# Kernel tuning notes

Hardware: AMD Instinct MI355X
Metric: run time of the kernel (lower is better)

The kernel has to match this reference:

```python
import jax, jax.numpy as jnp
import numpy as np

NUM_HEADS = 4

def setup_inputs() -> dict:
    key = jax.random.key(0)
    ks = jax.random.split(key, 5)
    B, T, F, C = 2, 128, 256, 256
    # weights scaled ~1/sqrt(C) so softmax is not saturated
    s = 1.0 / np.sqrt(C)
    return {
        "x": jax.random.normal(ks[0], (B, T, F, C), jnp.float32),
        "w_in": jax.random.normal(ks[1], (3 * C, C), jnp.float32) * s,
        "b_in": jax.random.normal(ks[2], (3 * C,), jnp.float32) * 0.01,
        "w_out": jax.random.normal(ks[3], (C, C), jnp.float32) * s,
        "b_out": jax.random.normal(ks[4], (C,), jnp.float32) * 0.01,
        "band": 16,
    }

def reference(x, w_in, b_in, w_out, b_out, band):
    B, T, F, C = x.shape
    H = NUM_HEADS
    D = C // H
    x2 = x.reshape(B * T, F, C)  # attention over frequency, independent per (B,T)
    qkv = x2 @ w_in.T + b_in  # [BT, F, 3C]
    q, k, v = jnp.split(qkv, 3, axis=-1)
    def heads(t):
        return t.reshape(B * T, F, H, D).transpose(0, 2, 1, 3)  # [BT, H, F, D]
    q, k, v = heads(q), heads(k), heads(v)
    scores = jnp.einsum('bhid,bhjd->bhij', q, k) / jnp.sqrt(jnp.asarray(D, x.dtype))
    i = jnp.arange(F)[:, None]
    j = jnp.arange(F)[None, :]
    keep = jnp.abs(i - j) <= band  # banded locality mask [F, F]
    scores = jnp.where(keep, scores, -jnp.inf)
    attn = jax.nn.softmax(scores, axis=-1)
    out = jnp.einsum('bhij,bhjd->bhid', attn, v)  # [BT, H, F, D]
    out = out.transpose(0, 2, 1, 3).reshape(B * T, F, C)
    y = out @ w_out.T + b_out
    return y.reshape(B, T, F, C)
```

## Files before the change

kernel.cpp:

```cpp
#include <hip/hip_runtime.h>
#include <hip/hip_bf16.h>
#include <cstdint>

typedef unsigned int u32;
typedef __attribute__((ext_vector_type(8))) __bf16 bf16x8;
typedef __attribute__((ext_vector_type(4))) float f32x4;
typedef __attribute__((ext_vector_type(2))) _Float16 half2_t;
typedef __attribute__((ext_vector_type(4))) _Float16 half4;
typedef __attribute__((ext_vector_type(2))) __fp16 fp16x2;

#define BT_N 256
#define F_N 256
#define C_N 256
#define H_N 4
#define D_N 64
#define TC_N 768
#define M_N (BT_N * F_N)
#define VT_ST 268

__device__ __forceinline__ ushort f2bf(float f) {
  u32 u = __float_as_uint(f);
  u32 r = (u + 0x7fffu + ((u >> 16) & 1u)) >> 16;
  return (ushort)r;
}

__device__ __forceinline__ void gload_lds16(const ushort* g, ushort* l) {
  __builtin_amdgcn_global_load_lds(
      (const __attribute__((address_space(1))) u32*)g,
      (__attribute__((address_space(3))) u32*)l, 16, 0, 0);
}

__global__ __launch_bounds__(256) void cvt3_f32_bf16_k(
    const float* __restrict__ sx, ushort* __restrict__ dx, int nx4,
    const float* __restrict__ si, ushort* __restrict__ di, int ni4,
    const float* __restrict__ so, ushort* __restrict__ dq, int no4) {
  int idx = blockIdx.x * 256 + threadIdx.x;
  int stride = gridDim.x * 256;
  int ntot = nx4 + ni4 + no4;
  for (int i = idx; i < ntot; i += stride) {
    const float4* s;
    ushort* d;
    if (i < nx4) { s = (const float4*)sx + i; d = dx + (size_t)i * 4; }
    else if (i < nx4 + ni4) { int k = i - nx4; s = (const float4*)si + k; d = di + (size_t)k * 4; }
    else { int k = i - nx4 - ni4; s = (const float4*)so + k; d = dq + (size_t)k * 4; }
    float4 v = *s;
    u32 a = (u32)f2bf(v.x) | ((u32)f2bf(v.y) << 16);
    u32 b = (u32)f2bf(v.z) | ((u32)f2bf(v.w) << 16);
    *(uint2*)d = make_uint2(a, b);
  }
}

template <typename OutT>
__global__ __launch_bounds__(256, 2) void gemm_bt(
    const ushort* __restrict__ Ap, const ushort* __restrict__ Bp,
    const float* __restrict__ bias, OutT* __restrict__ Cp,
    int N, int NTN, int nwg8) {
  constexpr bool F32OUT = (sizeof(OutT) == 4);
  constexpr int SMEM_BYTES = F32OUT ? 67584 : 65536;
  __shared__ char smem[SMEM_BYTES];
  ushort* smemH = (ushort*)smem;

  const int tid = threadIdx.x;
  const int lane = tid & 63;
  const int wid = tid >> 6;
  const int wr = wid >> 1, wc = wid & 1;
  const int l15 = lane & 15, l4 = lane >> 4;
  const int b = blockIdx.x;
  const int bid = (b & 7) * nwg8 + (b >> 3);
  const int tm = bid / NTN;
  const int tn = bid - tm * NTN;
  const int rowBase = tm * 128, colBase = tn * 128;

  f32x4 acc[4][4] = {};

  const int ar = (tid >> 3);
  const int akk = (((tid & 7) ^ (ar & 7)) << 3);
  const ushort* gA = Ap + (size_t)(rowBase + ar) * 256 + akk;
  const ushort* gB = Bp + (size_t)(colBase + ar) * 256 + akk;

#define STAGE(buf, k0)                                                        \
  {                                                                           \
    ushort* As_ = smemH + (buf) * 8192;                                       \
    ushort* Bs_ = smemH + 16384 + (buf) * 8192;                               \
    _Pragma("unroll") for (int c = 0; c < 4; ++c) {                           \
      gload_lds16(gA + (size_t)(c * 32) * 256 + (k0),                         \
                  As_ + (size_t)(c * 256 + (wid << 6)) * 8);                  \
      gload_lds16(gB + (size_t)(c * 32) * 256 + (k0),                         \
                  Bs_ + (size_t)(c * 256 + (wid << 6)) * 8);                  \
    }                                                                         \
  }

  STAGE(0, 0);
  int cur = 0;
#pragma unroll
  for (int t = 0; t < 4; ++t) {
    __syncthreads();
    if (t < 3) STAGE(cur ^ 1, (t + 1) * 64);
    const ushort* As_ = smemH + cur * 8192;
    const ushort* Bs_ = smemH + 16384 + cur * 8192;
#pragma unroll
    for (int kk = 0; kk < 2; ++kk) {
      bf16x8 af[4];
      bf16x8 bfr[4];
#pragma unroll
      for (int i2 = 0; i2 < 4; ++i2) {
        int row = wr * 64 + i2 * 16 + l15;
        af[i2] = *(const bf16x8*)(As_ + row * 64 + (((kk * 4 + l4) ^ (l15 & 7)) * 8));
      }
#pragma unroll
      for (int j2 = 0; j2 < 4; ++j2) {
        int row = wc * 64 + j2 * 16 + l15;
        bfr[j2] = *(const bf16x8*)(Bs_ + row * 64 + (((kk * 4 + l4) ^ (l15 & 7)) * 8));
      }
#pragma unroll
      for (int i2 = 0; i2 < 4; ++i2)
#pragma unroll
        for (int j2 = 0; j2 < 4; ++j2)
          acc[i2][j2] = __builtin_amdgcn_mfma_f32_16x16x32_bf16(
              af[i2], bfr[j2], acc[i2][j2], 0, 0, 0);
    }
    cur ^= 1;
  }
#undef STAGE

  __syncthreads();
  if constexpr (F32OUT) {
    float* eb = (float*)smem;
#pragma unroll
    for (int j2 = 0; j2 < 4; ++j2) {
      float bv = bias[colBase + wc * 64 + j2 * 16 + l15];
#pragma unroll
      for (int i2 = 0; i2 < 4; ++i2)
#pragma unroll
        for (int r = 0; r < 4; ++r)
          eb[(wr * 64 + i2 * 16 + l4 * 4 + r) * 132 + wc * 64 + j2 * 16 + l15] =
              acc[i2][j2][r] + bv;
    }
    __syncthreads();
#pragma unroll
    for (int i = 0; i < 32; ++i) {
      int row = wid * 32 + i;
      uint2 d = *(const uint2*)((const u32*)eb + row * 132 + lane * 2);
      *(uint2*)((float*)Cp + (size_t)(rowBase + row) * N + colBase + lane * 2) = d;
    }
  } else {
    ushort* eb = smemH;
#pragma unroll
    for (int j2 = 0; j2 < 4; ++j2) {
      float bv = bias[colBase + wc * 64 + j2 * 16 + l15];
#pragma unroll
      for (int i2 = 0; i2 < 4; ++i2)
#pragma unroll
        for (int r = 0; r < 4; ++r) {
          _Float16 h = (_Float16)(acc[i2][j2][r] + bv);
          eb[(wr * 64 + i2 * 16 + l4 * 4 + r) * 136 + wc * 64 + j2 * 16 + l15] =
              __builtin_bit_cast(ushort, h);
        }
    }
    __syncthreads();
#pragma unroll
    for (int i = 0; i < 16; ++i) {
      int row = wid * 32 + 2 * i + (lane >> 5);
      int hl = lane & 31;
      uint2 d = *(const uint2*)(eb + row * 136 + hl * 4);
      *(uint2*)((_Float16*)Cp + (size_t)(rowBase + row) * N + colBase + hl * 4) = d;
    }
  }
}

__global__ __launch_bounds__(256) void attn_mfma(
    const _Float16* __restrict__ qkv, ushort* __restrict__ aout) {
  __shared__ ushort smem[18432 + 64 * VT_ST];
  const int tid = threadIdx.x;
  const int bt = blockIdx.x >> 2;
  const int h = blockIdx.x & 3;
  const _Float16* base = qkv + (size_t)bt * 256 * 768 + h * 64;
  ushort* klds = smem;
  ushort* vlds = smem + 18432;

  {
    const int r0 = tid >> 3, c8 = tid & 7;
#pragma unroll
    for (int p = 0; p < 8; ++p) {
      int j = p * 32 + r0;
      const uint4 k4 = *(const uint4*)(base + (size_t)j * 768 + 256 + c8 * 8);
      *(uint4*)(klds + j * 72 + c8 * 8) = k4;
      const uint4 v4 = *(const uint4*)(base + (size_t)j * 768 + 512 + c8 * 8);
      const ushort* vh = (const ushort*)&v4;
      ushort* vtp = vlds + (c8 * 8) * VT_ST + j;
#pragma unroll
      for (int i = 0; i < 8; ++i) vtp[i * VT_ST] = vh[i];
    }
  }

  const int w = tid >> 6, lane = tid & 63;
  const int l15 = lane & 15, g = lane >> 4, g4 = g * 4;

  uint2 qf0[4], qf1[4], qf2[4], qf3[4];
  {
    const uint2* q0 = (const uint2*)(base + (size_t)(w * 64 + 0 * 16 + l15) * 768 + g4);
    const uint2* q1 = (const uint2*)(base + (size_t)(w * 64 + 1 * 16 + l15) * 768 + g4);
    const uint2* q2 = (const uint2*)(base + (size_t)(w * 64 + 2 * 16 + l15) * 768 + g4);
    const uint2* q3 = (const uint2*)(base + (size_t)(w * 64 + 3 * 16 + l15) * 768 + g4);
#pragma unroll
    for (int ks = 0; ks < 4; ++ks) {
      qf0[ks] = q0[ks * 4]; qf1[ks] = q1[ks * 4];
      qf2[ks] = q2[ks * 4]; qf3[ks] = q3[ks * 4];
    }
  }

  u32 bb = 0;
#pragma unroll
  for (int jt = 0; jt < 3; ++jt)
#pragma unroll
    for (int r = 0; r < 4; ++r) {
      int d = 16 * jt + g4 + r - 16 - l15;
      if (d >= -16 && d <= 16) bb |= 1u << (jt * 4 + r);
    }

  __syncthreads();

  const float SC = 0.18033688f;

#pragma unroll
  for (int rt = 0; rt < 4; ++rt) {
    const int R0 = w * 64 + rt * 16;
    const int Jc = R0 - 16;
    const uint2* qf = (rt == 0) ? qf0 : (rt == 1) ? qf1 : (rt == 2) ? qf2 : qf3;

    f32x4 st[3] = {};
#pragma unroll
    for (int jt = 0; jt < 3; ++jt) {
      int krow = Jc + 16 * jt + l15;
      krow = krow < 0 ? 0 : (krow > 255 ? 255 : krow);
      const ushort* kp = klds + krow * 72 + g4;
#pragma unroll
      for (int ks = 0; ks < 4; ++ks) {
        uint2 kf = *(const uint2*)(kp + ks * 16);
        st[jt] = __builtin_amdgcn_mfma_f32_16x16x16f16(
            __builtin_bit_cast(half4, kf), __builtin_bit_cast(half4, qf[ks]),
            st[jt], 0, 0, 0);
      }
    }

    float l_acc = 0.f;
    float pp[3][4];
#pragma unroll
    for (int jt = 0; jt < 3; ++jt)
#pragma unroll
      for (int r = 0; r < 4; ++r) {
        int jg = Jc + 16 * jt + g4 + r;
        bool keep = (((bb >> (jt * 4 + r)) & 1u) != 0) && (jg >= 0) && (jg < 256);
        float pv = keep ? __builtin_amdgcn_exp2f(st[jt][r] * SC) : 0.f;
        pp[jt][r] = pv;
        l_acc += pv;
      }
    l_acc += __shfl_xor(l_acc, 16, 64);
    l_acc += __shfl_xor(l_acc, 32, 64);
    const float inv = 1.f / l_acc;

    uint2 pf[3];
#pragma unroll
    for (int jt = 0; jt < 3; ++jt) {
      fp16x2 a = __builtin_amdgcn_cvt_pkrtz(pp[jt][0] * inv, pp[jt][1] * inv);
      fp16x2 c = __builtin_amdgcn_cvt_pkrtz(pp[jt][2] * inv, pp[jt][3] * inv);
      pf[jt].x = __builtin_bit_cast(u32, a);
      pf[jt].y = __builtin_bit_cast(u32, c);
    }

    f32x4 ot[4] = {};
#pragma unroll
    for (int kt = 0; kt < 3; ++kt) {
      int jb = Jc + 16 * kt + g4;
      jb = jb < 0 ? 0 : (jb > 252 ? 252 : jb);
#pragma unroll
      for (int mt = 0; mt < 4; ++mt) {
        uint2 vfr = *(const uint2*)(vlds + (16 * mt + l15) * VT_ST + jb);
        ot[mt] = __builtin_amdgcn_mfma_f32_16x16x16f16(
            __builtin_bit_cast(half4, vfr), __builtin_bit_cast(half4, pf[kt]),
            ot[mt], 0, 0, 0);
      }
    }

    ushort* orow = aout + (size_t)(bt * 256 + R0 + l15) * 256 + h * 64 + g4;
#pragma unroll
    for (int mt = 0; mt < 4; ++mt) {
      u32 lo = (u32)f2bf(ot[mt][0]) | ((u32)f2bf(ot[mt][1]) << 16);
      u32 hi = (u32)f2bf(ot[mt][2]) | ((u32)f2bf(ot[mt][3]) << 16);
      *(uint2*)(orow + mt * 16) = make_uint2(lo, hi);
    }
  }
}

extern "C" void kernel_launch(void* const* d_in, const int* in_sizes, int n_in,
                              void* d_out, int out_size, void* d_ws, size_t ws_size,
                              hipStream_t stream) {
  const float* x = (const float*)d_in[0];
  const float* w_in = (const float*)d_in[1];
  const float* b_in = (const float*)d_in[2];
  const float* w_out = (const float*)d_in[3];
  const float* b_out = (const float*)d_in[4];
  float* y = (float*)d_out;

  char* ws = (char*)d_ws;
  const size_t qkv_bytes = (size_t)M_N * TC_N * 2;
  const size_t xb_bytes = (size_t)M_N * C_N * 2;
  _Float16* qkv = (_Float16*)ws;
  ushort* xb = (ushort*)(ws + qkv_bytes);
  ushort* attn = xb;
  ushort* winb = (ushort*)(ws + qkv_bytes + xb_bytes);
  ushort* woutb = winb + TC_N * C_N;

  cvt3_f32_bf16_k<<<2048, 256, 0, stream>>>(x, xb, M_N * C_N / 4,
                                            w_in, winb, TC_N * C_N / 4,
                                            w_out, woutb, C_N * C_N / 4);

  gemm_bt<_Float16><<<(M_N / 128) * (TC_N / 128), 256, 0, stream>>>(
      xb, winb, b_in, qkv, TC_N, TC_N / 128, (M_N / 128) * (TC_N / 128) / 8);

  attn_mfma<<<BT_N * H_N, 256, 0, stream>>>(qkv, attn);

  gemm_bt<float><<<(M_N / 128) * (C_N / 128), 256, 0, stream>>>(
      attn, woutb, b_out, y, C_N, C_N / 128, (M_N / 128) * (C_N / 128) / 8);
}
```

Measured before the change: 102.9 us.

## Fuse input f32-to-bf16 conversion into QKV GEMM A-tile loading

The QKV projection GEMM now reads the f32 input directly and converts it to bf16 in registers before writing to shared memory, instead of relying on a separate conversion pass over x. The conversion kernel now only handles the weights. This removes one full read and write pass over the large activation tensor plus a bf16 intermediate buffer. In exchange, A-tile loads go through registers rather than direct global-to-LDS loads, which can increase register pressure and reduce overlap, and f32 A data is re-read across the column tiles.

```diff
diff --git a/kernel.cpp b/kernel.cpp
--- a/kernel.cpp
+++ b/kernel.cpp
@@ -24,35 +24,32 @@
   return (ushort)r;
 }
 
+__device__ __forceinline__ u32 pkbf(float a, float b) {
+  return (u32)f2bf(a) | ((u32)f2bf(b) << 16);
+}
+
 __device__ __forceinline__ void gload_lds16(const ushort* g, ushort* l) {
   __builtin_amdgcn_global_load_lds(
       (const __attribute__((address_space(1))) u32*)g,
       (__attribute__((address_space(3))) u32*)l, 16, 0, 0);
 }
 
-__global__ __launch_bounds__(256) void cvt3_f32_bf16_k(
-    const float* __restrict__ sx, ushort* __restrict__ dx, int nx4,
-    const float* __restrict__ si, ushort* __restrict__ di, int ni4,
-    const float* __restrict__ so, ushort* __restrict__ dq, int no4) {
+__global__ __launch_bounds__(256) void cvt2_f32_bf16_k(
+    const float* __restrict__ s0, ushort* __restrict__ d0, int n0,
+    const float* __restrict__ s1, ushort* __restrict__ d1, int n1) {
   int idx = blockIdx.x * 256 + threadIdx.x;
   int stride = gridDim.x * 256;
-  int ntot = nx4 + ni4 + no4;
-  for (int i = idx; i < ntot; i += stride) {
-    const float4* s;
-    ushort* d;
-    if (i < nx4) { s = (const float4*)sx + i; d = dx + (size_t)i * 4; }
-    else if (i < nx4 + ni4) { int k = i - nx4; s = (const float4*)si + k; d = di + (size_t)k * 4; }
-    else { int k = i - nx4 - ni4; s = (const float4*)so + k; d = dq + (size_t)k * 4; }
+  for (int i = idx; i < n0 + n1; i += stride) {
+    const float4* s = (i < n0) ? ((const float4*)s0 + i) : ((const float4*)s1 + (i - n0));
+    ushort* d = (i < n0) ? (d0 + (size_t)i * 4) : (d1 + (size_t)(i - n0) * 4);
     float4 v = *s;
-    u32 a = (u32)f2bf(v.x) | ((u32)f2bf(v.y) << 16);
-    u32 b = (u32)f2bf(v.z) | ((u32)f2bf(v.w) << 16);
-    *(uint2*)d = make_uint2(a, b);
-  }
-}
-
-template <typename OutT>
+    *(uint2*)d = make_uint2(pkbf(v.x, v.y), pkbf(v.z, v.w));
+  }
+}
+
+template <bool AF32, typename OutT>
 __global__ __launch_bounds__(256, 2) void gemm_bt(
-    const ushort* __restrict__ Ap, const ushort* __restrict__ Bp,
+    const void* __restrict__ Ap, const ushort* __restrict__ Bp,
     const float* __restrict__ bias, OutT* __restrict__ Cp,
     int N, int NTN, int nwg8) {
   constexpr bool F32OUT = (sizeof(OutT) == 4);
@@ -74,28 +71,66 @@
   f32x4 acc[4][4] = {};
 
   const int ar = (tid >> 3);
-  const int akk = (((tid & 7) ^ (ar & 7)) << 3);
-  const ushort* gA = Ap + (size_t)(rowBase + ar) * 256 + akk;
+  const int c8 = tid & 7;
+  const int akk = ((c8 ^ (ar & 7)) << 3);
   const ushort* gB = Bp + (size_t)(colBase + ar) * 256 + akk;
-
-#define STAGE(buf, k0)                                                        \
+  const ushort* gAh = (const ushort*)Ap + (size_t)(rowBase + ar) * 256 + akk;
+  const float* gAf = (const float*)Ap + (size_t)(rowBase + ar) * 256 + c8 * 8;
+
+  float4 a0[4], a1[4];
+
+#define STAGE_B(buf, k0)                                                      \
+  {                                                                           \
+    ushort* Bs_ = smemH + 16384 + (buf) * 8192;                               \
+    _Pragma("unroll") for (int c = 0; c < 4; ++c)                             \
+      gload_lds16(gB + (size_t)(c * 32) * 256 + (k0),                         \
+                  Bs_ + (size_t)(c * 256 + (wid << 6)) * 8);                  \
+  }
+#define STAGE_A16(buf, k0)                                                    \
   {                                                                           \
     ushort* As_ = smemH + (buf) * 8192;                                       \
-    ushort* Bs_ = smemH + 16384 + (buf) * 8192;                               \
+    _Pragma("unroll") for (int c = 0; c < 4; ++c)                             \
+      gload_lds16(gAh + (size_t)(c * 32) * 256 + (k0),                        \
+                  As_ + (size_t)(c * 256 + (wid << 6)) * 8);                  \
+  }
+#define LOAD_AF(k0)                                                           \
+  {                                                                           \
     _Pragma("unroll") for (int c = 0; c < 4; ++c) {                           \
-      gload_lds16(gA + (size_t)(c * 32) * 256 + (k0),                         \
-                  As_ + (size_t)(c * 256 + (wid << 6)) * 8);                  \
-      gload_lds16(gB + (size_t)(c * 32) * 256 + (k0),                         \
-                  Bs_ + (size_t)(c * 256 + (wid << 6)) * 8);                  \
+      const float* ga = gAf + (size_t)(c * 32) * 256 + (k0);                  \
+      a0[c] = *(const float4*)ga;                                             \
+      a1[c] = *(const float4*)(ga + 4);                                       \
     }                                                                         \
   }
-
-  STAGE(0, 0);
+#define WRITE_AF(buf)                                                         \
+  {                                                                           \
+    ushort* As_ = smemH + (buf) * 8192;                                       \
+    _Pragma("unroll") for (int c = 0; c < 4; ++c) {                           \
+      int row = ar + 32 * c;                                                  \
+      u32 p0 = pkbf(a0[c].x, a0[c].y), p1 = pkbf(a0[c].z, a0[c].w);           \
+      u32 p2 = pkbf(a1[c].x, a1[c].y), p3 = pkbf(a1[c].z, a1[c].w);           \
+      *(uint4*)(As_ + row * 64 + ((c8 ^ (ar & 7)) * 8)) =                     \
+          make_uint4(p0, p1, p2, p3);                                         \
+    }                                                                         \
+  }
+
+  if constexpr (AF32) {
+    LOAD_AF(0);
+    STAGE_B(0, 0);
+    WRITE_AF(0);
+  } else {
+    STAGE_A16(0, 0);
+    STAGE_B(0, 0);
+  }
+
   int cur = 0;
 #pragma unroll
   for (int t = 0; t < 4; ++t) {
     __syncthreads();
-    if (t < 3) STAGE(cur ^ 1, (t + 1) * 64);
+    if (t < 3) {
+      if constexpr (AF32) { LOAD_AF((t + 1) * 64); }
+      else { STAGE_A16(cur ^ 1, (t + 1) * 64); }
+      STAGE_B(cur ^ 1, (t + 1) * 64);
+    }
     const ushort* As_ = smemH + cur * 8192;
     const ushort* Bs_ = smemH + 16384 + cur * 8192;
 #pragma unroll
@@ -119,9 +154,15 @@
           acc[i2][j2] = __builtin_amdgcn_mfma_f32_16x16x32_bf16(
               af[i2], bfr[j2], acc[i2][j2], 0, 0, 0);
     }
+    if constexpr (AF32) {
+      if (t < 3) WRITE_AF(cur ^ 1);
+    }
     cur ^= 1;
   }
-#undef STAGE
+#undef STAGE_B
+#undef STAGE_A16
+#undef LOAD_AF
+#undef WRITE_AF
 
   __syncthreads();
   if constexpr (F32OUT) {
@@ -304,22 +345,19 @@
 
   char* ws = (char*)d_ws;
   const size_t qkv_bytes = (size_t)M_N * TC_N * 2;
-  const size_t xb_bytes = (size_t)M_N * C_N * 2;
   _Float16* qkv = (_Float16*)ws;
-  ushort* xb = (ushort*)(ws + qkv_bytes);
-  ushort* attn = xb;
-  ushort* winb = (ushort*)(ws + qkv_bytes + xb_bytes);
+  ushort* attn = (ushort*)(ws + qkv_bytes);
+  ushort* winb = attn + (size_t)M_N * C_N;
   ushort* woutb = winb + TC_N * C_N;
 
-  cvt3_f32_bf16_k<<<2048, 256, 0, stream>>>(x, xb, M_N * C_N / 4,
-                                            w_in, winb, TC_N * C_N / 4,
-                                            w_out, woutb, C_N * C_N / 4);
-
-  gemm_bt<_Float16><<<(M_N / 128) * (TC_N / 128), 256, 0, stream>>>(
-      xb, winb, b_in, qkv, TC_N, TC_N / 128, (M_N / 128) * (TC_N / 128) / 8);
+  cvt2_f32_bf16_k<<<256, 256, 0, stream>>>(w_in, winb, TC_N * C_N / 4,
+                                           w_out, woutb, C_N * C_N / 4);
+
+  gemm_bt<true, _Float16><<<(M_N / 128) * (TC_N / 128), 256, 0, stream>>>(
+      x, winb, b_in, qkv, TC_N, TC_N / 128, (M_N / 128) * (TC_N / 128) / 8);
 
   attn_mfma<<<BT_N * H_N, 256, 0, stream>>>(qkv, attn);
 
-  gemm_bt<float><<<(M_N / 128) * (C_N / 128), 256, 0, stream>>>(
+  gemm_bt<false, float><<<(M_N / 128) * (C_N / 128), 256, 0, stream>>>(
       attn, woutb, b_out, y, C_N, C_N / 128, (M_N / 128) * (C_N / 128) / 8);
 }
```

Result: slower. 114.9 us (+11.6%).
